# Kernel optimization log

Measured on AMD Instinct MI355X. Metric: run time of the kernel, lower is better.

The kernel has to match this reference:

```python
import jax, jax.numpy as jnp
import numpy as np

L, D, H, HD, M = 4096, 1024, 16, 64, 4096
EPS = 1e-5


def setup_inputs() -> dict:
    key = jax.random.key(0)
    ks = jax.random.split(key, 12)
    hidden_states = jax.random.normal(ks[0], (L, D), dtype=jnp.float32)
    cu_seqlens = jnp.arange(5, dtype=jnp.int32) * (L // 4)  # [0,1024,2048,3072,4096]
    # rope freqs as cos/sin of random angles: (L, HD//2, 2)
    angles = jax.random.uniform(ks[1], (L, HD // 2), dtype=jnp.float32) * (2.0 * np.pi)
    rope_freqs = jnp.stack([jnp.cos(angles), jnp.sin(angles)], axis=-1)
    s = 0.02
    params = {
        "ln0_g": jnp.ones((D,), jnp.float32), "ln0_b": jnp.zeros((D,), jnp.float32),
        "ln1_g": jnp.ones((D,), jnp.float32), "ln1_b": jnp.zeros((D,), jnp.float32),
        "w_qkv": jax.random.normal(ks[2], (D, 3 * D), jnp.float32) * s,
        "w_o":   jax.random.normal(ks[3], (D, D), jnp.float32) * s,
        "w_fc0": jax.random.normal(ks[4], (D, M), jnp.float32) * s,
        "b_fc0": jnp.zeros((M,), jnp.float32),
        "w_fc1": jax.random.normal(ks[5], (M, D), jnp.float32) * s,
        "b_fc1": jnp.zeros((D,), jnp.float32),
    }
    return {"hidden_states": hidden_states, "cu_seqlens": cu_seqlens, "rope_freqs": rope_freqs, **params}


def _layernorm(x, g, b):
    mu = jnp.mean(x, axis=-1, keepdims=True)
    var = jnp.var(x, axis=-1, keepdims=True)
    return (x - mu) * jax.lax.rsqrt(var + EPS) * g + b


def _apply_rope(x, fc):
    # x: (L, H, HD); fc: (L, HD//2, 2) -> broadcast over heads
    xr = x.reshape(L, H, HD // 2, 2)
    a, b = xr[..., 0], xr[..., 1]
    c, s = fc[:, None, :, 0], fc[:, None, :, 1]
    out = jnp.stack([a * c - b * s, a * s + b * c], axis=-1)
    return out.reshape(L, H, HD)


def reference(hidden_states, cu_seqlens, rope_freqs, ln0_g, ln0_b, ln1_g, ln1_b,
              w_qkv, w_o, w_fc0, b_fc0, w_fc1, b_fc1):
    residual = hidden_states
    x = _layernorm(hidden_states, ln0_g, ln0_b)
    qkv = (x @ w_qkv).reshape(L, 3, H, HD)
    q, k, v = qkv[:, 0], qkv[:, 1], qkv[:, 2]
    q = _apply_rope(q, rope_freqs)
    k = _apply_rope(k, rope_freqs)
    # block-diagonal mask from cu_seqlens
    seg = jnp.searchsorted(cu_seqlens[1:], jnp.arange(L, dtype=cu_seqlens.dtype), side="right")
    mask = seg[:, None] == seg[None, :]  # (L, L)
    scale = 1.0 / np.sqrt(HD)
    scores = jnp.einsum("lhd,mhd->hlm", q, k) * scale
    scores = jnp.where(mask[None], scores, jnp.float32(-1e30))
    probs = jax.nn.softmax(scores, axis=-1)
    attn = jnp.einsum("hlm,mhd->lhd", probs, v).reshape(L, D)
    attn = attn @ w_o
    h = residual + attn
    y = _layernorm(h, ln1_g, ln1_b)
    y = jax.nn.gelu(y @ w_fc0 + b_fc0, approximate=False) @ w_fc1 + b_fc1
    return h + y
```

## Files before the change

### kernel.cpp

```cpp
#include <hip/hip_runtime.h>
#include <cstdint>
#include <cmath>

#define L_ 4096
#define D_ 1024
#define H_ 16
#define HD_ 64
#define M_ 4096

typedef __bf16 bf16_t;
typedef __attribute__((ext_vector_type(8))) __bf16 bf16x8;
typedef __attribute__((ext_vector_type(4))) __bf16 bf16x4;
typedef __attribute__((ext_vector_type(4))) float f32x4;

#define WAIT_VM0 0x0f70
#define WAIT_LGKM0 0xc07f

__device__ __forceinline__ f32x4 mfma16(bf16x8 a, bf16x8 b, f32x4 c) {
    return __builtin_amdgcn_mfma_f32_16x16x32_bf16(a, b, c, 0, 0, 0);
}

__device__ __forceinline__ void gload_lds16(const bf16_t* g, bf16_t* l) {
    __builtin_amdgcn_global_load_lds(
        (const __attribute__((address_space(1))) unsigned int*)(g),
        (__attribute__((address_space(3))) unsigned int*)(l), 16, 0, 0);
}

__device__ __forceinline__ float fast_exp2(float x) {
    float r;
    asm volatile("v_exp_f32 %0, %1" : "=v"(r) : "v"(x));
    return r;
}
__device__ __forceinline__ float fast_rcp(float x) {
    float r;
    asm volatile("v_rcp_f32 %0, %1" : "=v"(r) : "v"(x));
    return r;
}
__device__ __forceinline__ float gelu_f(float v) {
    float t = v * (0.7978845608f + 0.0356774081f * v * v);
    return v * fast_rcp(1.f + fast_exp2(-2.885390082f * t));
}

__global__ __launch_bounds__(256) void ln_kernel(const float* __restrict__ x,
                                                 const float* __restrict__ g,
                                                 const float* __restrict__ b,
                                                 bf16_t* __restrict__ out) {
    int row = blockIdx.x, tid = threadIdx.x;
    int wave = tid >> 6, lane = tid & 63;
    const f32x4* xr = (const f32x4*)(x + (long)row * D_);
    f32x4 v = xr[tid];
    float s = v.x + v.y + v.z + v.w;
    __shared__ float red[8];
#pragma unroll
    for (int off = 32; off > 0; off >>= 1) s += __shfl_down(s, off, 64);
    if (lane == 0) red[wave] = s;
    __syncthreads();
    float mean = (red[0] + red[1] + red[2] + red[3]) * (1.f / 1024.f);
    float s2 = 0.f;
#pragma unroll
    for (int i = 0; i < 4; i++) { float d = v[i] - mean; s2 += d * d; }
#pragma unroll
    for (int off = 32; off > 0; off >>= 1) s2 += __shfl_down(s2, off, 64);
    __syncthreads();
    if (lane == 0) red[wave] = s2;
    __syncthreads();
    float var = (red[0] + red[1] + red[2] + red[3]) * (1.f / 1024.f);
    float rstd = rsqrtf(var + 1e-5f);
    f32x4 g4 = ((const f32x4*)g)[tid];
    f32x4 b4 = ((const f32x4*)b)[tid];
    bf16x4 o;
#pragma unroll
    for (int i = 0; i < 4; i++) o[i] = (bf16_t)((v[i] - mean) * rstd * g4[i] + b4[i]);
    *(bf16x4*)(out + (long)row * D_ + tid * 4) = o;
}

__global__ __launch_bounds__(256) void transpose_all(
    const float* __restrict__ w_qkv, const float* __restrict__ w_o,
    const float* __restrict__ w_fc0, const float* __restrict__ w_fc1,
    bf16_t* __restrict__ t_qkv, bf16_t* __restrict__ t_o,
    bf16_t* __restrict__ t_fc0, bf16_t* __restrict__ t_fc1) {
    __shared__ float t[32][33];
    int bidx = blockIdx.x;
    const float* W;
    bf16_t* Wt;
    int K, N, tile;
    if (bidx < 3072) { W = w_qkv; Wt = t_qkv; K = 1024; N = 3072; tile = bidx; }
    else if (bidx < 4096) { W = w_o; Wt = t_o; K = 1024; N = 1024; tile = bidx - 3072; }
    else if (bidx < 8192) { W = w_fc0; Wt = t_fc0; K = 1024; N = 4096; tile = bidx - 4096; }
    else { W = w_fc1; Wt = t_fc1; K = 4096; N = 1024; tile = bidx - 8192; }
    int nt = N >> 5;
    int n0 = (tile % nt) * 32, k0 = (tile / nt) * 32;
    int tx = threadIdx.x & 31, ty = threadIdx.x >> 5;
#pragma unroll
    for (int r = 0; r < 32; r += 8)
        t[ty + r][tx] = W[(long)(k0 + ty + r) * N + n0 + tx];
    __syncthreads();
#pragma unroll
    for (int r = 0; r < 32; r += 8)
        Wt[(long)(n0 + ty + r) * K + k0 + tx] = (bf16_t)t[tx][ty + r];
}

__global__ __launch_bounds__(256) void vt_kernel(const bf16_t* __restrict__ qkv,
                                                 bf16_t* __restrict__ Vt) {
    __shared__ bf16_t t[32][33];
    int l0 = blockIdx.x * 32, c0 = blockIdx.y * 32;
    int tx = threadIdx.x & 31, ty = threadIdx.x >> 5;
#pragma unroll
    for (int r = 0; r < 32; r += 8)
        t[ty + r][tx] = qkv[(long)(l0 + ty + r) * 3072 + 2048 + c0 + tx];
    __syncthreads();
#pragma unroll
    for (int r = 0; r < 32; r += 8)
        Vt[(long)(c0 + ty + r) * 4096 + l0 + tx] = t[tx][ty + r];
}

__global__ __launch_bounds__(256) void rope_kernel(bf16_t* __restrict__ qkv,
                                                   const float* __restrict__ freqs) {
    const float k1 = 0.125f * 1.44269504089f;
    int idx = blockIdx.x * 256 + threadIdx.x;
    int g = idx & 7;
    int h = (idx >> 3) & 15;
    int l = idx >> 7;
    const float* f = freqs + (long)l * 64 + g * 8;
    f32x4 f0 = ((const f32x4*)f)[0];
    f32x4 f1 = ((const f32x4*)f)[1];
    float c[4] = {f0.x, f0.z, f1.x, f1.z};
    float s[4] = {f0.y, f0.w, f1.y, f1.w};
    bf16_t* qp = qkv + (long)l * 3072 + h * 64 + g * 8;
    bf16x8 q = *(bf16x8*)qp;
    bf16x8 k = *(bf16x8*)(qp + 1024);
    bf16x8 qo, ko;
#pragma unroll
    for (int e = 0; e < 4; e++) {
        float a = (float)q[2 * e], b = (float)q[2 * e + 1];
        qo[2 * e] = (bf16_t)((a * c[e] - b * s[e]) * k1);
        qo[2 * e + 1] = (bf16_t)((a * s[e] + b * c[e]) * k1);
        a = (float)k[2 * e]; b = (float)k[2 * e + 1];
        ko[2 * e] = (bf16_t)(a * c[e] - b * s[e]);
        ko[2 * e + 1] = (bf16_t)(a * s[e] + b * c[e]);
    }
    *(bf16x8*)qp = qo;
    *(bf16x8*)(qp + 1024) = ko;
}

#define STAGE_A(d, h, kt)                                                          \
    gload_lds16(aSt + (long)((h) * 128) * K + (kt), &SA[d][h][(wv * 16) * 64]);    \
    gload_lds16(aSt + (long)((h) * 128 + 8) * K + (kt), &SA[d][h][(wv * 16 + 8) * 64]);

#define STAGE_B(d, h, kt)                                                          \
    gload_lds16(bSt + (long)((h) * 128) * K + (kt), &SB[d][h][(wv * 16) * 64]);    \
    gload_lds16(bSt + (long)((h) * 128 + 8) * K + (kt), &SB[d][h][(wv * 16 + 8) * 64]);

#define RD_A(dst, src, rq)                                                          \
    _Pragma("unroll") for (int i_ = 0; i_ < 4; i_++) {                              \
        dst[i_][0] = *(const bf16x8*)&src[((rq) * 64 + i_ * 16 + l16) * 64 + sl0 * 8]; \
        dst[i_][1] = *(const bf16x8*)&src[((rq) * 64 + i_ * 16 + l16) * 64 + sl1 * 8]; \
    }

#define RD_B(dst, src, cq)                                                          \
    _Pragma("unroll") for (int j_ = 0; j_ < 2; j_++) {                              \
        dst[j_][0] = *(const bf16x8*)&src[(bro + (cq) * 32 + j_ * 16 + l16) * 64 + sl0 * 8]; \
        dst[j_][1] = *(const bf16x8*)&src[(bro + (cq) * 32 + j_ * 16 + l16) * 64 + sl1 * 8]; \
    }

#define MFMA_Q(rq, cq, Af, Bf)                                                      \
    _Pragma("unroll") for (int i_ = 0; i_ < 4; i_++)                                \
    _Pragma("unroll") for (int j_ = 0; j_ < 2; j_++) {                              \
        acc[(rq) * 4 + i_][(cq) * 2 + j_] =                                         \
            mfma16(Af[i_][0], Bf[j_][0], acc[(rq) * 4 + i_][(cq) * 2 + j_]);        \
        acc[(rq) * 4 + i_][(cq) * 2 + j_] =                                         \
            mfma16(Af[i_][1], Bf[j_][1], acc[(rq) * 4 + i_][(cq) * 2 + j_]);        \
    }

#define LGKM0() asm volatile("s_waitcnt lgkmcnt(0)" ::: "memory")
#define VMC(n) asm volatile("s_waitcnt vmcnt(" #n ")" ::: "memory")
#define BAR() __builtin_amdgcn_s_barrier()
#define PRIO1() __builtin_amdgcn_s_setprio(1)
#define PRIO0() __builtin_amdgcn_s_setprio(0)

template <int EPI>
__device__ __forceinline__ void gemm256_core(
    const bf16_t* __restrict__ A, const bf16_t* __restrict__ Bt,
    int K, int N, long bm, long bn, int kb, int ke,
    bf16_t* __restrict__ outB, const float* __restrict__ bias) {
    __shared__ __align__(16) bf16_t SA[2][2][128 * 64];
    __shared__ __align__(16) bf16_t SB[2][2][128 * 64];
    int tid = threadIdx.x;
    int wv = tid >> 6, lane = tid & 63;
    int quad = lane >> 4, l16 = lane & 15;
    int wm = wv >> 2, wn = wv & 3;
    int lr = lane >> 3;
    int sc = (lane & 7) ^ (lr & 7);
    int sl0 = quad ^ (l16 & 7);
    int sl1 = (4 + quad) ^ (l16 & 7);
    int bro = (wn & 1) * 64;

    const bf16_t* aSt = A + (bm + wv * 16 + lr) * (long)K + sc * 8;
    const bf16_t* bSt = Bt + (bn + wv * 16 + lr) * (long)K + sc * 8;
    const bf16_t* pa0 = SA[0][wm];
    const bf16_t* pa1 = SA[1][wm];
    const bf16_t* pb0 = SB[0][wn >> 1];
    const bf16_t* pb1 = SB[1][wn >> 1];

    f32x4 acc[8][4];
#pragma unroll
    for (int i = 0; i < 8; i++)
#pragma unroll
        for (int j = 0; j < 4; j++) acc[i][j] = (f32x4){0.f, 0.f, 0.f, 0.f};

    bf16x8 a0[4][2], a1[4][2], b0[2][2], b1[2][2];

    STAGE_B(0, 0, kb); STAGE_B(0, 1, kb); STAGE_A(0, 0, kb); STAGE_A(0, 1, kb);
    STAGE_B(1, 0, kb + 64); STAGE_B(1, 1, kb + 64);
    STAGE_A(1, 0, kb + 64); STAGE_A(1, 1, kb + 64);
    VMC(8);
    BAR();
    RD_A(a0, pa0, 0); RD_B(b0, pb0, 0); RD_B(b1, pb0, 1);
    LGKM0();

    for (int k0 = kb; k0 < ke; k0 += 128) {
        int kt2 = (k0 + 128 < ke) ? k0 + 128 : kb;
        int kt3 = kt2 + 64;
        BAR(); STAGE_B(0, 0, kt2); STAGE_B(0, 1, kt2);
        PRIO1(); MFMA_Q(0, 0, a0, b0); MFMA_Q(0, 1, a0, b1); PRIO0();
        RD_A(a1, pa0, 1); LGKM0();
        VMC(4);
        BAR(); STAGE_A(0, 0, kt2); STAGE_A(0, 1, kt2);
        PRIO1(); MFMA_Q(1, 0, a1, b0); MFMA_Q(1, 1, a1, b1); PRIO0();
        RD_A(a0, pa1, 0); RD_B(b0, pb1, 0); RD_B(b1, pb1, 1); LGKM0();
        BAR(); STAGE_B(1, 0, kt3); STAGE_B(1, 1, kt3);
        PRIO1(); MFMA_Q(0, 0, a0, b0); MFMA_Q(0, 1, a0, b1); PRIO0();
        RD_A(a1, pa1, 1); LGKM0();
        VMC(4);
        BAR(); STAGE_A(1, 0, kt3); STAGE_A(1, 1, kt3);
        PRIO1(); MFMA_Q(1, 0, a1, b0); MFMA_Q(1, 1, a1, b1); PRIO0();
        RD_A(a0, pa0, 0); RD_B(b0, pb0, 0); RD_B(b1, pb0, 1); LGKM0();
    }
    VMC(0);

#pragma unroll
    for (int ri = 0; ri < 8; ri++)
#pragma unroll
        for (int cj = 0; cj < 4; cj++)
#pragma unroll
            for (int r = 0; r < 4; r++) {
                long row = bm + wm * 128 + (ri >> 2) * 64 + (ri & 3) * 16 + quad * 4 + r;
                long col = bn + wn * 64 + (cj >> 1) * 32 + (cj & 1) * 16 + l16;
                long idx = row * (long)N + col;
                float v = acc[ri][cj][r];
                if (EPI == 0) {
                    outB[idx] = (bf16_t)v;
                } else {
                    v += bias[col];
                    outB[idx] = (bf16_t)gelu_f(v);
                }
            }
}

__global__ __launch_bounds__(512) void gemm256_qkv(const bf16_t* __restrict__ A,
                                                   const bf16_t* __restrict__ Bt,
                                                   bf16_t* __restrict__ outB) {
    int g = blockIdx.x & 7, w = blockIdx.x >> 3;
    int gm = g >> 2, gn = g & 3;
    long bm = (long)(gm * 8 + w / 3) * 256;
    long bn = (long)(gn * 3 + w % 3) * 256;
    gemm256_core<0>(A, Bt, 1024, 3072, bm, bn, 0, 1024, outB, nullptr);
}

__global__ __launch_bounds__(512) void gemm256_fc0(const bf16_t* __restrict__ A,
                                                   const bf16_t* __restrict__ Bt,
                                                   bf16_t* __restrict__ outB,
                                                   const float* __restrict__ bias) {
    int g = blockIdx.x & 7, w = blockIdx.x >> 3;
    int gm = g >> 2, gn = g & 3;
    long bm = (long)(gm * 8 + (w >> 2)) * 256;
    long bn = (long)(gn * 4 + (w & 3)) * 256;
    gemm256_core<2>(A, Bt, 1024, 4096, bm, bn, 0, 1024, outB, bias);
}

__global__ __launch_bounds__(512) void gemm256_fc1(const bf16_t* __restrict__ A,
                                                   const bf16_t* __restrict__ Bt,
                                                   bf16_t* __restrict__ P) {
    int g = blockIdx.x & 7, w = blockIdx.x >> 3;
    int z = g >> 1, gm = g & 1;
    long bm = (long)(gm * 8 + (w >> 2)) * 256;
    long bn = (long)(w & 3) * 256;
    gemm256_core<0>(A, Bt, 4096, 1024, bm, bn, z * 1024, z * 1024 + 1024,
                    P + (long)z * L_ * D_, nullptr);
}

__global__ __launch_bounds__(256) void reduce_fc1(const bf16_t* __restrict__ P,
                                                  const float* __restrict__ bias,
                                                  float* __restrict__ out) {
    long i = (long)blockIdx.x * 256 + threadIdx.x;
    f32x4 b = ((const f32x4*)bias)[i & 255];
    f32x4 v = ((f32x4*)out)[i];
#pragma unroll
    for (int z = 0; z < 4; z++) {
        bf16x4 p = ((const bf16x4*)(P + (long)z * L_ * D_))[i];
#pragma unroll
        for (int e = 0; e < 4; e++) v[e] += (float)p[e];
    }
    v.x += b.x; v.y += b.y; v.z += b.z; v.w += b.w;
    ((f32x4*)out)[i] = v;
}

__global__ __launch_bounds__(256) void gemm_bt64_res(const bf16_t* __restrict__ A,
                                                     const bf16_t* __restrict__ Bt,
                                                     int M, int N, int K,
                                                     float* __restrict__ outF,
                                                     const float* __restrict__ res) {
    __shared__ __align__(16) bf16_t As[128 * 64];
    __shared__ __align__(16) bf16_t Bs[64 * 64];
    int tid = threadIdx.x;
    int wave = tid >> 6, lane = tid & 63;
    int quad = lane >> 4, l16 = lane & 15;

    int g = blockIdx.x & 7, w = blockIdx.x >> 3;
    int bn_i = w & 15, bm_i = g * 4 + (w >> 4);
    long bm = (long)bm_i * 128, bn = (long)bn_i * 64;

    f32x4 acc[2][4];
#pragma unroll
    for (int i = 0; i < 2; i++)
#pragma unroll
        for (int j = 0; j < 4; j++) acc[i][j] = (f32x4){0.f, 0.f, 0.f, 0.f};

    int lr = lane >> 3;
    int sc = (lane & 7) ^ (lr & 7);
    const bf16_t* a_base = A + (bm + wave * 32 + lr) * (long)K + sc * 8;
    const bf16_t* b_base = Bt + (bn + wave * 16 + lr) * (long)K + sc * 8;

    for (int k0 = 0; k0 < K; k0 += 64) {
        __syncthreads();
#pragma unroll
        for (int i = 0; i < 4; i++)
            gload_lds16(a_base + k0 + (long)(8 * i) * K, &As[(wave * 32 + 8 * i) * 64]);
#pragma unroll
        for (int i = 0; i < 2; i++)
            gload_lds16(b_base + k0 + (long)(8 * i) * K, &Bs[(wave * 16 + 8 * i) * 64]);
        __builtin_amdgcn_s_waitcnt(WAIT_VM0);
        __syncthreads();

#pragma unroll
        for (int h = 0; h < 2; h++) {
            int sl = (h * 4 + quad) ^ (l16 & 7);
            bf16x8 af[2], bfr[4];
#pragma unroll
            for (int i = 0; i < 2; i++)
                af[i] = *(const bf16x8*)&As[(wave * 32 + i * 16 + l16) * 64 + sl * 8];
#pragma unroll
            for (int j = 0; j < 4; j++)
                bfr[j] = *(const bf16x8*)&Bs[(j * 16 + l16) * 64 + sl * 8];
#pragma unroll
            for (int i = 0; i < 2; i++)
#pragma unroll
                for (int j = 0; j < 4; j++)
                    acc[i][j] = mfma16(af[i], bfr[j], acc[i][j]);
        }
    }

#pragma unroll
    for (int i = 0; i < 2; i++)
#pragma unroll
        for (int j = 0; j < 4; j++)
#pragma unroll
            for (int r = 0; r < 4; r++) {
                long row = bm + wave * 32 + i * 16 + quad * 4 + r;
                long col = bn + j * 16 + l16;
                long idx = row * (long)N + col;
                outF[idx] = acc[i][j][r] + res[idx];
            }
}

__global__ __launch_bounds__(256) void attn_kernel(const bf16_t* __restrict__ qkv,
                                                   const bf16_t* __restrict__ Vt,
                                                   const int* __restrict__ cu,
                                                   bf16_t* __restrict__ out) {
    __shared__ __align__(16) bf16_t QPs[4 * 16 * 72];
    __shared__ __align__(16) bf16_t Ks[2][64 * 64];
    __shared__ __align__(16) bf16_t Vs[2][64 * 64];

    int tid = threadIdx.x, wave = tid >> 6, lane = tid & 63;
    int quad = lane >> 4, l16 = lane & 15;

    int g = blockIdx.x & 7, w = blockIdx.x >> 3;
    int head = (w & 1) * 8 + g;
    int qt = (w >> 1) & 15;
    int seg = w >> 5;
    int s0 = cu[seg], s1 = cu[seg + 1];
    int r0 = s0 + qt * 64;
    const long hoff = (long)head * 64;

    bf16_t* Qs = QPs;
    bf16_t* Psw = &QPs[wave * 16 * 72];

    int lr = lane >> 3;
    int sc = (lane & 7) ^ (lr & 7);
    int sl0 = (0 * 4 + quad) ^ (l16 & 7);
    int sl1 = (1 * 4 + quad) ^ (l16 & 7);

#pragma unroll
    for (int i = 0; i < 2; i++) {
        int row = wave * 16 + i * 8 + lr;
        gload_lds16(qkv + (long)(r0 + row) * 3072 + hoff + sc * 8,
                    &Qs[(wave * 16 + i * 8) * 64]);
    }
#pragma unroll
    for (int tp = 0; tp < 2; tp++) {
#pragma unroll
        for (int i = 0; i < 2; i++) {
            int row = wave * 16 + i * 8 + lr;
            long kt = s0 + tp * 64;
            gload_lds16(qkv + (kt + row) * (long)3072 + 1024 + hoff + sc * 8,
                        &Ks[tp][(wave * 16 + i * 8) * 64]);
            gload_lds16(Vt + (hoff + row) * (long)4096 + kt + sc * 8,
                        &Vs[tp][(wave * 16 + i * 8) * 64]);
        }
    }
    VMC(8);
    BAR();
    bf16x8 aq0 = *(const bf16x8*)&Qs[(wave * 16 + l16) * 64 + sl0 * 8];
    bf16x8 aq1 = *(const bf16x8*)&Qs[(wave * 16 + l16) * 64 + sl1 * 8];

    bf16x8 ones;
#pragma unroll
    for (int e = 0; e < 8; e++) ones[e] = (bf16_t)1.0f;

    f32x4 o[4];
#pragma unroll
    for (int j = 0; j < 4; j++) o[j] = (f32x4){0.f, 0.f, 0.f, 0.f};
    f32x4 lacc = (f32x4){0.f, 0.f, 0.f, 0.f};

    int nt = (s1 - s0) >> 6;
    for (int t = 0; t < nt; t++) {
        int cur = t & 1;
        VMC(4);
        BAR();

        f32x4 sacc[4];
#pragma unroll
        for (int j = 0; j < 4; j++) sacc[j] = (f32x4){0.f, 0.f, 0.f, 0.f};
#pragma unroll
        for (int j = 0; j < 4; j++) {
            bf16x8 b0 = *(const bf16x8*)&Ks[cur][(j * 16 + l16) * 64 + sl0 * 8];
            bf16x8 b1 = *(const bf16x8*)&Ks[cur][(j * 16 + l16) * 64 + sl1 * 8];
            sacc[j] = mfma16(aq0, b0, sacc[j]);
            sacc[j] = mfma16(aq1, b1, sacc[j]);
        }

#pragma unroll
        for (int j = 0; j < 4; j++)
#pragma unroll
            for (int r = 0; r < 4; r++)
                Psw[(quad * 4 + r) * 72 + j * 16 + l16] = (bf16_t)fast_exp2(sacc[j][r]);

        __builtin_amdgcn_s_waitcnt(WAIT_LGKM0);

        bf16x8 ap0 = *(const bf16x8*)&Psw[l16 * 72 + 0 * 32 + quad * 8];
        bf16x8 ap1 = *(const bf16x8*)&Psw[l16 * 72 + 1 * 32 + quad * 8];
#pragma unroll
        for (int j2 = 0; j2 < 4; j2++) {
            bf16x8 b0 = *(const bf16x8*)&Vs[cur][(j2 * 16 + l16) * 64 + sl0 * 8];
            bf16x8 b1 = *(const bf16x8*)&Vs[cur][(j2 * 16 + l16) * 64 + sl1 * 8];
            o[j2] = mfma16(ap0, b0, o[j2]);
            o[j2] = mfma16(ap1, b1, o[j2]);
        }
        lacc = mfma16(ap0, ones, lacc);
        lacc = mfma16(ap1, ones, lacc);

        BAR();
        int t2 = (t + 2 < nt) ? t + 2 : t;
        long kt2 = s0 + (long)t2 * 64;
#pragma unroll
        for (int i = 0; i < 2; i++) {
            int row = wave * 16 + i * 8 + lr;
            gload_lds16(qkv + (kt2 + row) * (long)3072 + 1024 + hoff + sc * 8,
                        &Ks[cur][(wave * 16 + i * 8) * 64]);
            gload_lds16(Vt + (hoff + row) * (long)4096 + kt2 + sc * 8,
                        &Vs[cur][(wave * 16 + i * 8) * 64]);
        }
    }
    VMC(0);

#pragma unroll
    for (int r = 0; r < 4; r++) {
        float inv = fast_rcp(lacc[r]);
        int row = r0 + wave * 16 + quad * 4 + r;
#pragma unroll
        for (int j2 = 0; j2 < 4; j2++)
            out[(long)row * 1024 + head * 64 + j2 * 16 + l16] = (bf16_t)(o[j2][r] * inv);
    }
}

extern "C" void kernel_launch(void* const* d_in, const int* in_sizes, int n_in,
                              void* d_out, int out_size, void* d_ws, size_t ws_size,
                              hipStream_t stream) {
    const float* hidden = (const float*)d_in[0];
    const int* cu = (const int*)d_in[1];
    const float* freqs = (const float*)d_in[2];
    const float* ln0_g = (const float*)d_in[3];
    const float* ln0_b = (const float*)d_in[4];
    const float* ln1_g = (const float*)d_in[5];
    const float* ln1_b = (const float*)d_in[6];
    const float* w_qkv = (const float*)d_in[7];
    const float* w_o = (const float*)d_in[8];
    const float* w_fc0 = (const float*)d_in[9];
    const float* b_fc0 = (const float*)d_in[10];
    const float* w_fc1 = (const float*)d_in[11];
    const float* b_fc1 = (const float*)d_in[12];
    float* out = (float*)d_out;

    char* ws = (char*)d_ws;
    bf16_t* qkv = (bf16_t*)(ws);
    bf16_t* attn = (bf16_t*)(ws + ((size_t)24 << 20));
    bf16_t* act = (bf16_t*)(ws);
    bf16_t* x_bf = (bf16_t*)(ws + ((size_t)32 << 20));
    bf16_t* Vt = x_bf;
    bf16_t* y_bf = x_bf;
    bf16_t* fc1p = (bf16_t*)(ws + ((size_t)40 << 20));
    bf16_t* wqkvT = (bf16_t*)(ws + ((size_t)72 << 20));
    bf16_t* woT = (bf16_t*)(ws + ((size_t)78 << 20));
    bf16_t* wfc0T = (bf16_t*)(ws + ((size_t)80 << 20));
    bf16_t* wfc1T = (bf16_t*)(ws + ((size_t)88 << 20));
    float* h = out;

    transpose_all<<<12288, 256, 0, stream>>>(w_qkv, w_o, w_fc0, w_fc1,
                                             wqkvT, woT, wfc0T, wfc1T);

    ln_kernel<<<L_, 256, 0, stream>>>(hidden, ln0_g, ln0_b, x_bf);

    gemm256_qkv<<<192, 512, 0, stream>>>(x_bf, wqkvT, qkv);

    rope_kernel<<<(L_ * H_ * 8) / 256, 256, 0, stream>>>(qkv, freqs);
    vt_kernel<<<dim3(4096 / 32, 1024 / 32), 256, 0, stream>>>(qkv, Vt);

    attn_kernel<<<1024, 256, 0, stream>>>(qkv, Vt, cu, attn);

    gemm_bt64_res<<<512, 256, 0, stream>>>(
        attn, woT, L_, 1024, 1024, h, hidden);

    ln_kernel<<<L_, 256, 0, stream>>>(h, ln1_g, ln1_b, y_bf);

    gemm256_fc0<<<256, 512, 0, stream>>>(y_bf, wfc0T, act, b_fc0);

    gemm256_fc1<<<256, 512, 0, stream>>>(act, wfc1T, fc1p);
    reduce_fc1<<<(L_ * D_ / 4) / 256, 256, 0, stream>>>(fc1p, b_fc1, out);
}
```

Before: 315.0 us.

## Software-pipeline QK^T one tile ahead of softmax and PV in attention

Computes the score tile for the next K block while the exp/PV work of the current block runs, keeping two score accumulators (sA/sB). K loads are issued earlier, right after the first barrier, since the current K buffer is no longer needed once the previous iteration consumed it. V loads stay after the PV barrier, and the wait counts are adjusted. This adds register pressure from the extra accumulators and relies on the split K/V load timing and vmcnt values being correct.

After: 312.0 us. Within noise of the previous version (-1.0%).

```diff
diff --git a/kernel.cpp b/kernel.cpp
--- a/kernel.cpp
+++ b/kernel.cpp
@@ -432,28 +432,48 @@
     for (int j = 0; j < 4; j++) o[j] = (f32x4){0.f, 0.f, 0.f, 0.f};
     f32x4 lacc = (f32x4){0.f, 0.f, 0.f, 0.f};
 
+    VMC(6);
+    BAR();
+    f32x4 sA[4], sB[4];
+#pragma unroll
+    for (int j = 0; j < 4; j++) {
+        sA[j] = (f32x4){0.f, 0.f, 0.f, 0.f};
+        bf16x8 b0 = *(const bf16x8*)&Ks[0][(j * 16 + l16) * 64 + sl0 * 8];
+        bf16x8 b1 = *(const bf16x8*)&Ks[0][(j * 16 + l16) * 64 + sl1 * 8];
+        sA[j] = mfma16(aq0, b0, sA[j]);
+        sA[j] = mfma16(aq1, b1, sA[j]);
+    }
+
     int nt = (s1 - s0) >> 6;
     for (int t = 0; t < nt; t++) {
-        int cur = t & 1;
-        VMC(4);
+        int cur = t & 1, nxt = (t + 1) & 1;
+        int tK = (t + 2 < nt) ? t + 2 : t;
+        long ktn = s0 + (long)tK * 64;
+
+        VMC(2);
         BAR();
 
-        f32x4 sacc[4];
-#pragma unroll
-        for (int j = 0; j < 4; j++) sacc[j] = (f32x4){0.f, 0.f, 0.f, 0.f};
+#pragma unroll
+        for (int i = 0; i < 2; i++) {
+            int row = wave * 16 + i * 8 + lr;
+            gload_lds16(qkv + (ktn + row) * (long)3072 + 1024 + hoff + sc * 8,
+                        &Ks[cur][(wave * 16 + i * 8) * 64]);
+        }
+
 #pragma unroll
         for (int j = 0; j < 4; j++) {
-            bf16x8 b0 = *(const bf16x8*)&Ks[cur][(j * 16 + l16) * 64 + sl0 * 8];
-            bf16x8 b1 = *(const bf16x8*)&Ks[cur][(j * 16 + l16) * 64 + sl1 * 8];
-            sacc[j] = mfma16(aq0, b0, sacc[j]);
-            sacc[j] = mfma16(aq1, b1, sacc[j]);
+            sB[j] = (f32x4){0.f, 0.f, 0.f, 0.f};
+            bf16x8 b0 = *(const bf16x8*)&Ks[nxt][(j * 16 + l16) * 64 + sl0 * 8];
+            bf16x8 b1 = *(const bf16x8*)&Ks[nxt][(j * 16 + l16) * 64 + sl1 * 8];
+            sB[j] = mfma16(aq0, b0, sB[j]);
+            sB[j] = mfma16(aq1, b1, sB[j]);
         }
 
 #pragma unroll
         for (int j = 0; j < 4; j++)
 #pragma unroll
             for (int r = 0; r < 4; r++)
-                Psw[(quad * 4 + r) * 72 + j * 16 + l16] = (bf16_t)fast_exp2(sacc[j][r]);
+                Psw[(quad * 4 + r) * 72 + j * 16 + l16] = (bf16_t)fast_exp2(sA[j][r]);
 
         __builtin_amdgcn_s_waitcnt(WAIT_LGKM0);
 
@@ -470,16 +490,15 @@
         lacc = mfma16(ap1, ones, lacc);
 
         BAR();
-        int t2 = (t + 2 < nt) ? t + 2 : t;
-        long kt2 = s0 + (long)t2 * 64;
 #pragma unroll
         for (int i = 0; i < 2; i++) {
             int row = wave * 16 + i * 8 + lr;
-            gload_lds16(qkv + (kt2 + row) * (long)3072 + 1024 + hoff + sc * 8,
-                        &Ks[cur][(wave * 16 + i * 8) * 64]);
-            gload_lds16(Vt + (hoff + row) * (long)4096 + kt2 + sc * 8,
+            gload_lds16(Vt + (hoff + row) * (long)4096 + ktn + sc * 8,
                         &Vs[cur][(wave * 16 + i * 8) * 64]);
         }
+
+#pragma unroll
+        for (int j = 0; j < 4; j++) sA[j] = sB[j];
     }
     VMC(0);
 
```

## Keep attention probabilities in registers by transposing S and permuting V layout

Applied to the files above, without the earlier changes.

The QK^T MFMA operands are swapped so the score tile is computed transposed, which lets each lane build the P operand for the PV MFMA directly from its accumulator registers after exp2. This removes the LDS round trip (store P, wait, reload) and the per-wave P staging buffer. To keep the reduction order consistent, the V-transpose kernel now writes columns in a permuted key order within each 64-row block. This couples the Vt layout to the register mapping, so any mismatch would silently corrupt the attention output.

Measured after the change: 299.9 us. 1.05x faster.

```diff
diff --git a/kernel.cpp b/kernel.cpp
--- a/kernel.cpp
+++ b/kernel.cpp
@@ -109,9 +109,14 @@
     for (int r = 0; r < 32; r += 8)
         t[ty + r][tx] = qkv[(long)(l0 + ty + r) * 3072 + 2048 + c0 + tx];
     __syncthreads();
+    int w64 = (l0 & 32) + tx;
+    int h = w64 >> 5, m = w64 & 31;
+    int a = m >> 2, v = m & 3;
+    int gp = 2 * (a & 3) + (a >> 2);
+    int wp = (l0 & ~63) + 32 * h + 4 * gp + v;
 #pragma unroll
     for (int r = 0; r < 32; r += 8)
-        Vt[(long)(c0 + ty + r) * 4096 + l0 + tx] = t[tx][ty + r];
+        Vt[(long)(c0 + ty + r) * 4096 + wp] = t[tx][ty + r];
 }
 
 __global__ __launch_bounds__(256) void rope_kernel(bf16_t* __restrict__ qkv,
@@ -377,7 +382,7 @@
                                                    const bf16_t* __restrict__ Vt,
                                                    const int* __restrict__ cu,
                                                    bf16_t* __restrict__ out) {
-    __shared__ __align__(16) bf16_t QPs[4 * 16 * 72];
+    __shared__ __align__(16) bf16_t Qs[64 * 64];
     __shared__ __align__(16) bf16_t Ks[2][64 * 64];
     __shared__ __align__(16) bf16_t Vs[2][64 * 64];
 
@@ -391,9 +396,6 @@
     int s0 = cu[seg], s1 = cu[seg + 1];
     int r0 = s0 + qt * 64;
     const long hoff = (long)head * 64;
-
-    bf16_t* Qs = QPs;
-    bf16_t* Psw = &QPs[wave * 16 * 72];
 
     int lr = lane >> 3;
     int sc = (lane & 7) ^ (lr & 7);
@@ -440,31 +442,27 @@
 
         f32x4 sacc[4];
 #pragma unroll
-        for (int j = 0; j < 4; j++) sacc[j] = (f32x4){0.f, 0.f, 0.f, 0.f};
-#pragma unroll
         for (int j = 0; j < 4; j++) {
-            bf16x8 b0 = *(const bf16x8*)&Ks[cur][(j * 16 + l16) * 64 + sl0 * 8];
-            bf16x8 b1 = *(const bf16x8*)&Ks[cur][(j * 16 + l16) * 64 + sl1 * 8];
-            sacc[j] = mfma16(aq0, b0, sacc[j]);
-            sacc[j] = mfma16(aq1, b1, sacc[j]);
+            sacc[j] = (f32x4){0.f, 0.f, 0.f, 0.f};
+            bf16x8 kb0 = *(const bf16x8*)&Ks[cur][(j * 16 + l16) * 64 + sl0 * 8];
+            bf16x8 kb1 = *(const bf16x8*)&Ks[cur][(j * 16 + l16) * 64 + sl1 * 8];
+            sacc[j] = mfma16(kb0, aq0, sacc[j]);
+            sacc[j] = mfma16(kb1, aq1, sacc[j]);
         }
 
-#pragma unroll
-        for (int j = 0; j < 4; j++)
-#pragma unroll
-            for (int r = 0; r < 4; r++)
-                Psw[(quad * 4 + r) * 72 + j * 16 + l16] = (bf16_t)fast_exp2(sacc[j][r]);
-
-        __builtin_amdgcn_s_waitcnt(WAIT_LGKM0);
-
-        bf16x8 ap0 = *(const bf16x8*)&Psw[l16 * 72 + 0 * 32 + quad * 8];
-        bf16x8 ap1 = *(const bf16x8*)&Psw[l16 * 72 + 1 * 32 + quad * 8];
+        bf16x8 ap0, ap1;
+#pragma unroll
+        for (int e = 0; e < 8; e++) {
+            ap0[e] = (bf16_t)fast_exp2(sacc[e >> 2][e & 3]);
+            ap1[e] = (bf16_t)fast_exp2(sacc[2 + (e >> 2)][e & 3]);
+        }
+
 #pragma unroll
         for (int j2 = 0; j2 < 4; j2++) {
-            bf16x8 b0 = *(const bf16x8*)&Vs[cur][(j2 * 16 + l16) * 64 + sl0 * 8];
-            bf16x8 b1 = *(const bf16x8*)&Vs[cur][(j2 * 16 + l16) * 64 + sl1 * 8];
-            o[j2] = mfma16(ap0, b0, o[j2]);
-            o[j2] = mfma16(ap1, b1, o[j2]);
+            bf16x8 bv0 = *(const bf16x8*)&Vs[cur][(j2 * 16 + l16) * 64 + sl0 * 8];
+            bf16x8 bv1 = *(const bf16x8*)&Vs[cur][(j2 * 16 + l16) * 64 + sl1 * 8];
+            o[j2] = mfma16(ap0, bv0, o[j2]);
+            o[j2] = mfma16(ap1, bv1, o[j2]);
         }
         lacc = mfma16(ap0, ones, lacc);
         lacc = mfma16(ap1, ones, lacc);
```
